# Optimization experiments

Hardware: AMD Instinct MI355X
Metric: run time of the kernel (lower is better)

Reference implementation:

```python
import jax, jax.numpy as jnp
import numpy as np

N = 50000
E = 600000
D = 128  # embedding_dimension


def _lrelu(x):
    return jax.nn.leaky_relu(x, negative_slope=0.01)


def _rgcn(x, edge_index, edge_type, rel_w, root_w, bias):
    # FastRGCNConv, num_relations=2, aggr='mean' (PyG default).
    # Compute per-relation transforms as 2 dense GEMMs, then gather per edge.
    h = jnp.einsum('nd,rde->rne', x, rel_w)          # [2, N, D]
    src, dst = edge_index[0], edge_index[1]
    msg = h[edge_type, src]                          # [E, D] gather
    agg = jax.ops.segment_sum(msg, dst, num_segments=x.shape[0])
    deg = jax.ops.segment_sum(jnp.ones((msg.shape[0],), x.dtype), dst,
                              num_segments=x.shape[0])
    agg = agg / jnp.maximum(deg, 1.0)[:, None]       # mean over in-edges
    return agg + x @ root_w + bias


def setup_inputs() -> dict:
    key = jax.random.key(0)
    ks = jax.random.split(key, 32)
    f32 = jnp.float32
    inp = {
        'des': jax.random.normal(ks[0], (N, 768), f32),
        'tweet': jax.random.normal(ks[1], (N, 768), f32),
        'num_prop': jax.random.normal(ks[2], (N, 7), f32),
        'cat_prop': jax.random.normal(ks[3], (N, 11), f32),
        'new_feature': jax.random.normal(ks[4], (N, 1), f32),
        'edge_index': jax.random.randint(ks[5], (2, E), 0, N),
        'edge_type': jax.random.randint(ks[6], (E,), 0, 2),
    }
    def lin(k, i, o, s=0.05):
        kw, kb = jax.random.split(k)
        return (jax.random.normal(kw, (i, o), f32) * s,
                jax.random.normal(kb, (o,), f32) * s)
    pf = D // 5  # 25
    inp['W_des'], inp['b_des'] = lin(ks[7], 768, pf)
    inp['W_tweet'], inp['b_tweet'] = lin(ks[8], 768, 28)
    inp['W_num'], inp['b_num'] = lin(ks[9], 7, pf)
    inp['W_cat'], inp['b_cat'] = lin(ks[10], 11, pf)
    inp['W_new'], inp['b_new'] = lin(ks[11], 1, pf)
    inp['W_in'], inp['b_in'] = lin(ks[12], D, D)
    inp['rel_w1'] = jax.random.normal(ks[13], (2, D, D), f32) * 0.05
    inp['root_w1'] = jax.random.normal(ks[14], (D, D), f32) * 0.05
    inp['bias1'] = jax.random.normal(ks[15], (D,), f32) * 0.05
    inp['rel_w2'] = jax.random.normal(ks[16], (2, D, D), f32) * 0.05
    inp['root_w2'] = jax.random.normal(ks[17], (D, D), f32) * 0.05
    inp['bias2'] = jax.random.normal(ks[18], (D,), f32) * 0.05
    inp['W_out1'], inp['b_out1'] = lin(ks[19], D, D)
    inp['W_out2'], inp['b_out2'] = lin(ks[20], D, 2)
    return inp


def reference(des, tweet, num_prop, cat_prop, new_feature,
              W_des, b_des, W_tweet, b_tweet, W_num, b_num,
              W_cat, b_cat, W_new, b_new, W_in, b_in,
              rel_w1, root_w1, bias1, rel_w2, root_w2, bias2,
              W_out1, b_out1, W_out2, b_out2,
              edge_index, edge_type):
    d = _lrelu(des @ W_des + b_des)
    t = _lrelu(tweet @ W_tweet + b_tweet)
    n = _lrelu(num_prop @ W_num + b_num)
    c = _lrelu(cat_prop @ W_cat + b_cat)
    nf = _lrelu(new_feature @ W_new + b_new)
    x = jnp.concatenate((d, t, n, c, nf), axis=1)  # [N, 128]
    x = _lrelu(x @ W_in + b_in)
    x = _rgcn(x, edge_index, edge_type, rel_w1, root_w1, bias1)
    # dropout is identity at eval time
    x = _rgcn(x, edge_index, edge_type, rel_w2, root_w2, bias2)
    x = _lrelu(x @ W_out1 + b_out1)
    return x @ W_out2 + b_out2  # [N, 2]
```

## Files before the change

kernel.cpp:

```cpp
#include <hip/hip_runtime.h>

#define N_NODES 50000
#define N_EDGES 600000
#define NPAD    50048
#define NBLK_SCAN 196

static __device__ __forceinline__ float lrelu(float v) {
    return v > 0.f ? v : 0.01f * v;
}

#define RS_P 129

template<int NC>
__device__ __forceinline__ void proj_lds_body(
    const float* __restrict__ A, const float* __restrict__ W,
    const float* __restrict__ bias, float* __restrict__ X0,
    int colbase, float* AlT)
{
    constexpr int CH = (NC + 1) / 2;
    const int t    = threadIdx.x;
    const int row  = t & 127;
    const int half = t >> 7;
    const int c0   = __builtin_amdgcn_readfirstlane(half ? (NC - CH) : 0);
    const int r0   = blockIdx.x * 128;
    const int q    = t & 7;

    float acc[CH];
    #pragma unroll
    for (int c = 0; c < CH; c++) acc[c] = 0.f;

    for (int k0 = 0; k0 < 768; k0 += 32) {
        __syncthreads();
        #pragma unroll
        for (int i = 0; i < 4; i++) {
            int rr = i * 32 + (t >> 3);
            int gr = r0 + rr;
            float4 v = make_float4(0.f, 0.f, 0.f, 0.f);
            if (gr < N_NODES)
                v = *(const float4*)&A[(size_t)gr * 768 + k0 + q * 4];
            AlT[(q * 4 + 0) * RS_P + rr] = v.x;
            AlT[(q * 4 + 1) * RS_P + rr] = v.y;
            AlT[(q * 4 + 2) * RS_P + rr] = v.z;
            AlT[(q * 4 + 3) * RS_P + rr] = v.w;
        }
        __syncthreads();
        const float* Wk = W + (size_t)k0 * NC + c0;
        #pragma unroll
        for (int k = 0; k < 32; k++) {
            float a = AlT[k * RS_P + row];
            const float* w = Wk + k * NC;
            #pragma unroll
            for (int c = 0; c < CH; c++) acc[c] += a * w[c];
        }
    }
    int grow = r0 + row;
    if (grow < N_NODES) {
        #pragma unroll
        for (int c = 0; c < CH; c++) {
            float v = lrelu(acc[c] + bias[c0 + c]);
            X0[(size_t)grow * 128 + colbase + c0 + c] = v;
        }
    }
}

__global__ __launch_bounds__(256) void proj768_lds(
    const float* __restrict__ des, const float* __restrict__ Wd, const float* __restrict__ bd,
    const float* __restrict__ tw,  const float* __restrict__ Wt, const float* __restrict__ bt,
    float* __restrict__ X0)
{
    __shared__ float AlT[32 * RS_P];
    if (blockIdx.z == 0) proj_lds_body<25>(des, Wd, bd, X0, 0,  AlT);
    else                 proj_lds_body<28>(tw, Wt, bt, X0, 25, AlT);
}

__global__ void small_proj_kernel(
    const float* __restrict__ nump, const float* __restrict__ catp, const float* __restrict__ newf,
    const float* __restrict__ Wn, const float* __restrict__ bn,
    const float* __restrict__ Wc, const float* __restrict__ bc,
    const float* __restrict__ Ww, const float* __restrict__ bw,
    float* __restrict__ out)
{
    int id = blockIdx.x * 256 + threadIdx.x;
    int n = id / 75, c = id % 75;
    if (n >= N_NODES) return;
    float acc; int col;
    if (c < 25) {
        col = 53 + c; acc = bn[c];
        #pragma unroll
        for (int k = 0; k < 7; k++) acc += nump[n * 7 + k] * Wn[k * 25 + c];
    } else if (c < 50) {
        int cc = c - 25; col = 78 + cc; acc = bc[cc];
        #pragma unroll
        for (int k = 0; k < 11; k++) acc += catp[n * 11 + k] * Wc[k * 25 + cc];
    } else {
        int cc = c - 50; col = 103 + cc;
        acc = bw[cc] + newf[n] * Ww[cc];
    }
    out[(size_t)n * 128 + col] = lrelu(acc);
}

template<int KTOT, bool SPLIT, bool ACT>
__global__ __launch_bounds__(256, 4) void gemm_v2(
    const float* __restrict__ A, const float* __restrict__ A2,
    const float* __restrict__ B, const float* __restrict__ B2,
    const float* __restrict__ bias, float* __restrict__ out)
{
    __shared__ float AlT[32 * 132];
    __shared__ float Bl [32 * 132];
    const int t  = threadIdx.x;
    const int r0 = blockIdx.x * 128;
    const int tx = t & 15, ty = t >> 4;

    float acc[8][8] = {};

    for (int k0 = 0; k0 < KTOT; k0 += 32) {
        #pragma unroll
        for (int i = 0; i < 4; i++) {
            int f4i = t + i * 256;
            int row = f4i >> 3, c4 = f4i & 7;
            int k = k0 + c4 * 4;
            float4 v;
            if (!SPLIT) {
                v = *(const float4*)&A[(size_t)(r0 + row) * 128 + k];
            } else {
                if (k < 256) v = *(const float4*)&A[(size_t)(r0 + row) * 256 + k];
                else         v = *(const float4*)&A2[(size_t)(r0 + row) * 128 + (k - 256)];
            }
            AlT[(c4 * 4 + 0) * 132 + row] = v.x;
            AlT[(c4 * 4 + 1) * 132 + row] = v.y;
            AlT[(c4 * 4 + 2) * 132 + row] = v.z;
            AlT[(c4 * 4 + 3) * 132 + row] = v.w;
        }
        #pragma unroll
        for (int i = 0; i < 4; i++) {
            int f4i = t + i * 256;
            int kk = f4i >> 5, c4 = f4i & 31;
            int k = k0 + kk;
            float4 v;
            if (!SPLIT) v = *(const float4*)&B[(size_t)k * 128 + c4 * 4];
            else v = (k < 256) ? *(const float4*)&B[(size_t)k * 128 + c4 * 4]
                               : *(const float4*)&B2[(size_t)(k - 256) * 128 + c4 * 4];
            *(float4*)&Bl[kk * 132 + c4 * 4] = v;
        }
        __syncthreads();
        #pragma unroll 4
        for (int k = 0; k < 32; k++) {
            float4 a0 = *(const float4*)&AlT[k * 132 + ty * 8];
            float4 a1 = *(const float4*)&AlT[k * 132 + ty * 8 + 4];
            float4 b0 = *(const float4*)&Bl [k * 132 + tx * 8];
            float4 b1 = *(const float4*)&Bl [k * 132 + tx * 8 + 4];
            float av[8] = {a0.x, a0.y, a0.z, a0.w, a1.x, a1.y, a1.z, a1.w};
            float bv[8] = {b0.x, b0.y, b0.z, b0.w, b1.x, b1.y, b1.z, b1.w};
            #pragma unroll
            for (int i = 0; i < 8; i++)
                #pragma unroll
                for (int j = 0; j < 8; j++) acc[i][j] += av[i] * bv[j];
        }
        __syncthreads();
    }
    float4 bb0 = *(const float4*)&bias[tx * 8];
    float4 bb1 = *(const float4*)&bias[tx * 8 + 4];
    float bb[8] = {bb0.x, bb0.y, bb0.z, bb0.w, bb1.x, bb1.y, bb1.z, bb1.w};
    #pragma unroll
    for (int i = 0; i < 8; i++) {
        size_t row = (size_t)(r0 + ty * 8 + i);
        float o[8];
        #pragma unroll
        for (int j = 0; j < 8; j++) {
            o[j] = acc[i][j] + bb[j];
            if (ACT) o[j] = lrelu(o[j]);
        }
        *(float4*)&out[row * 128 + tx * 8]     = make_float4(o[0], o[1], o[2], o[3]);
        *(float4*)&out[row * 128 + tx * 8 + 4] = make_float4(o[4], o[5], o[6], o[7]);
    }
}

__global__ void count_kernel(const int* __restrict__ ei, int* __restrict__ count) {
    int e = blockIdx.x * 256 + threadIdx.x;
    if (e < N_EDGES) atomicAdd(&count[ei[N_EDGES + e]], 1);
}

__global__ void scan1_kernel(const int* __restrict__ count, int* __restrict__ partial) {
    __shared__ int sm[256];
    int b = blockIdx.x, t = threadIdx.x;
    int i = b * 256 + t;
    sm[t] = (i < N_NODES) ? count[i] : 0;
    __syncthreads();
    for (int off = 128; off > 0; off >>= 1) {
        if (t < off) sm[t] += sm[t + off];
        __syncthreads();
    }
    if (t == 0) partial[b] = sm[0];
}

__global__ void scan2_kernel(int* __restrict__ partial) {
    __shared__ int sm[256];
    int t = threadIdx.x;
    int v = (t < NBLK_SCAN) ? partial[t] : 0;
    sm[t] = v; __syncthreads();
    for (int off = 1; off < 256; off <<= 1) {
        int add = (t >= off) ? sm[t - off] : 0;
        __syncthreads();
        sm[t] += add;
        __syncthreads();
    }
    partial[t] = sm[t] - v;
}

__global__ void scan3_kernel(const int* __restrict__ count, const int* __restrict__ partial,
                             int* __restrict__ offsets) {
    __shared__ int sm[256];
    int b = blockIdx.x, t = threadIdx.x;
    int i = b * 256 + t;
    int v = (i < N_NODES) ? count[i] : 0;
    sm[t] = v; __syncthreads();
    for (int off = 1; off < 256; off <<= 1) {
        int add = (t >= off) ? sm[t - off] : 0;
        __syncthreads();
        sm[t] += add;
        __syncthreads();
    }
    if (i < N_NODES) offsets[i] = partial[b] + sm[t] - v;
}

__global__ void fill_kernel(const int* __restrict__ ei, const int* __restrict__ et,
                            const int* __restrict__ offsets, int* __restrict__ cursor,
                            int* __restrict__ elist) {
    int e = blockIdx.x * 256 + threadIdx.x;
    if (e < N_EDGES) {
        int d = ei[N_EDGES + e];
        int pos = atomicAdd(&cursor[d], 1);
        elist[offsets[d] + pos] = (int)(((unsigned)ei[e]) | (((unsigned)et[e]) << 31));
    }
}

__global__ __launch_bounds__(256) void aggregate_v3(
    const float* __restrict__ x, const int* __restrict__ offsets,
    const int* __restrict__ count, const int* __restrict__ elist,
    float* __restrict__ s)
{
    int nid  = blockIdx.x * 8 + (threadIdx.x >> 5);
    int lane = threadIdx.x & 31;
    if (nid >= N_NODES) return;
    int start = offsets[nid], dg = count[nid];
    float4 a0 = make_float4(0.f, 0.f, 0.f, 0.f);
    float4 a1 = make_float4(0.f, 0.f, 0.f, 0.f);
    int i = 0;
    for (; i + 2 <= dg; i += 2) {
        int v0 = elist[start + i];
        int v1 = elist[start + i + 1];
        float4 u = ((const float4*)&x[(size_t)(v0 & 0x7FFFFFFF) * 128])[lane];
        float4 w = ((const float4*)&x[(size_t)(v1 & 0x7FFFFFFF) * 128])[lane];
        if (v0 < 0) { a1.x += u.x; a1.y += u.y; a1.z += u.z; a1.w += u.w; }
        else        { a0.x += u.x; a0.y += u.y; a0.z += u.z; a0.w += u.w; }
        if (v1 < 0) { a1.x += w.x; a1.y += w.y; a1.z += w.z; a1.w += w.w; }
        else        { a0.x += w.x; a0.y += w.y; a0.z += w.z; a0.w += w.w; }
    }
    if (i < dg) {
        int v0 = elist[start + i];
        float4 u = ((const float4*)&x[(size_t)(v0 & 0x7FFFFFFF) * 128])[lane];
        if (v0 < 0) { a1.x += u.x; a1.y += u.y; a1.z += u.z; a1.w += u.w; }
        else        { a0.x += u.x; a0.y += u.y; a0.z += u.z; a0.w += u.w; }
    }
    float inv = 1.0f / (float)(dg > 0 ? dg : 1);
    a0.x *= inv; a0.y *= inv; a0.z *= inv; a0.w *= inv;
    a1.x *= inv; a1.y *= inv; a1.z *= inv; a1.w *= inv;
    ((float4*)&s[(size_t)nid * 256])[lane]       = a0;
    ((float4*)&s[(size_t)nid * 256 + 128])[lane] = a1;
}

__global__ __launch_bounds__(64) void final_kernel(
    const float* __restrict__ x, const float* __restrict__ W2,
    const float* __restrict__ b2, float* __restrict__ out)
{
    int n = blockIdx.x;
    int t = threadIdx.x;
    float x0 = x[(size_t)n * 128 + t];
    float x1 = x[(size_t)n * 128 + 64 + t];
    float p0 = x0 * W2[t * 2]     + x1 * W2[(t + 64) * 2];
    float p1 = x0 * W2[t * 2 + 1] + x1 * W2[(t + 64) * 2 + 1];
    #pragma unroll
    for (int off = 32; off > 0; off >>= 1) {
        p0 += __shfl_down(p0, off);
        p1 += __shfl_down(p1, off);
    }
    if (t == 0) {
        out[(size_t)n * 2]     = p0 + b2[0];
        out[(size_t)n * 2 + 1] = p1 + b2[1];
    }
}

extern "C" void kernel_launch(void* const* d_in, const int* in_sizes, int n_in,
                              void* d_out, int out_size, void* d_ws, size_t ws_size,
                              hipStream_t stream)
{
    const float* des   = (const float*)d_in[0];
    const float* tw    = (const float*)d_in[1];
    const float* nump  = (const float*)d_in[2];
    const float* catp  = (const float*)d_in[3];
    const float* newf  = (const float*)d_in[4];
    const int*   ei    = (const int*)d_in[5];
    const int*   et    = (const int*)d_in[6];
    const float* Wd    = (const float*)d_in[7];  const float* bd  = (const float*)d_in[8];
    const float* Wt    = (const float*)d_in[9];  const float* bt  = (const float*)d_in[10];
    const float* Wn    = (const float*)d_in[11]; const float* bn  = (const float*)d_in[12];
    const float* Wc    = (const float*)d_in[13]; const float* bc  = (const float*)d_in[14];
    const float* Ww    = (const float*)d_in[15]; const float* bw  = (const float*)d_in[16];
    const float* Win   = (const float*)d_in[17]; const float* bin = (const float*)d_in[18];
    const float* relw1 = (const float*)d_in[19]; const float* rootw1 = (const float*)d_in[20];
    const float* bias1 = (const float*)d_in[21];
    const float* relw2 = (const float*)d_in[22]; const float* rootw2 = (const float*)d_in[23];
    const float* bias2 = (const float*)d_in[24];
    const float* Wo1   = (const float*)d_in[25]; const float* bo1 = (const float*)d_in[26];
    const float* Wo2   = (const float*)d_in[27]; const float* bo2 = (const float*)d_in[28];
    float* outp = (float*)d_out;

    char* ws = (char*)d_ws;
    const size_t szX = (size_t)NPAD * 128 * sizeof(float);
    float* X0 = (float*)(ws);
    float* X1 = (float*)(ws + szX);
    float* S  = (float*)(ws + 2 * szX);
    char* p = ws + 2 * szX + (size_t)NPAD * 256 * sizeof(float);
    int* count   = (int*)p; p += (size_t)NPAD * 4;
    int* offsets = (int*)p; p += (size_t)NPAD * 4;
    int* cursor  = (int*)p; p += (size_t)NPAD * 4;
    int* elist   = (int*)p; p += (size_t)N_EDGES * 4;
    int* partial = (int*)p;

    hipMemsetAsync(count,  0, NPAD * sizeof(int), stream);
    hipMemsetAsync(cursor, 0, NPAD * sizeof(int), stream);

    dim3 pg(NPAD / 128, 1, 2);
    proj768_lds<<<pg, 256, 0, stream>>>(des, Wd, bd, tw, Wt, bt, X0);
    small_proj_kernel<<<(N_NODES * 75 + 255) / 256, 256, 0, stream>>>(
        nump, catp, newf, Wn, bn, Wc, bc, Ww, bw, X0);
    gemm_v2<128, false, true><<<NPAD / 128, 256, 0, stream>>>(
        X0, nullptr, Win, nullptr, bin, X1);

    count_kernel<<<(N_EDGES + 255) / 256, 256, 0, stream>>>(ei, count);
    scan1_kernel<<<NBLK_SCAN, 256, 0, stream>>>(count, partial);
    scan2_kernel<<<1, 256, 0, stream>>>(partial);
    scan3_kernel<<<NBLK_SCAN, 256, 0, stream>>>(count, partial, offsets);
    fill_kernel<<<(N_EDGES + 255) / 256, 256, 0, stream>>>(ei, et, offsets, cursor, elist);

    aggregate_v3<<<(N_NODES + 7) / 8, 256, 0, stream>>>(X1, offsets, count, elist, S);
    gemm_v2<384, true, false><<<NPAD / 128, 256, 0, stream>>>(
        S, X1, relw1, rootw1, bias1, X0);

    aggregate_v3<<<(N_NODES + 7) / 8, 256, 0, stream>>>(X0, offsets, count, elist, S);
    gemm_v2<384, true, false><<<NPAD / 128, 256, 0, stream>>>(
        S, X0, relw2, rootw2, bias2, X1);

    gemm_v2<128, false, true><<<NPAD / 128, 256, 0, stream>>>(
        X1, nullptr, Wo1, nullptr, bo1, X0);
    final_kernel<<<N_NODES, 64, 0, stream>>>(X0, Wo2, bo2, outp);
}
```

Baseline: 953.8 us.

## Restructure 768-wide projection into per-wave tiles with split-K reduction

Replaces the block-wide LDS-transposed projection with a per-wave scheme: each wave owns 64 rows and half of K, stages its own tile in private LDS without block barriers, and computes all output columns per thread. The two K-halves are combined through LDS after a single barrier. This removes the per-tile __syncthreads, gives each thread more columns and better ILP from 8 outstanding float4 loads, at the cost of more accumulator registers and reading W twice as often per row.

Result: slower. 1.101 ms (+15.4%).

```diff
diff --git a/kernel.cpp b/kernel.cpp
--- a/kernel.cpp
+++ b/kernel.cpp
@@ -9,68 +9,80 @@
     return v > 0.f ? v : 0.01f * v;
 }
 
-#define RS_P 129
+#define PW_STRIDE 65
+#define PW_WORDS  (32 * PW_STRIDE)
 
 template<int NC>
-__device__ __forceinline__ void proj_lds_body(
+__device__ __forceinline__ void proj_wave_body(
     const float* __restrict__ A, const float* __restrict__ W,
     const float* __restrict__ bias, float* __restrict__ X0,
-    int colbase, float* AlT)
-{
-    constexpr int CH = (NC + 1) / 2;
-    const int t    = threadIdx.x;
-    const int row  = t & 127;
-    const int half = t >> 7;
-    const int c0   = __builtin_amdgcn_readfirstlane(half ? (NC - CH) : 0);
-    const int r0   = blockIdx.x * 128;
-    const int q    = t & 7;
-
-    float acc[CH];
+    int colbase, float* __restrict__ lbuf, float* __restrict__ pbuf,
+    int r0, int khalf, int lane)
+{
+    float acc[NC];
     #pragma unroll
-    for (int c = 0; c < CH; c++) acc[c] = 0.f;
-
-    for (int k0 = 0; k0 < 768; k0 += 32) {
-        __syncthreads();
-        #pragma unroll
-        for (int i = 0; i < 4; i++) {
-            int rr = i * 32 + (t >> 3);
-            int gr = r0 + rr;
-            float4 v = make_float4(0.f, 0.f, 0.f, 0.f);
-            if (gr < N_NODES)
-                v = *(const float4*)&A[(size_t)gr * 768 + k0 + q * 4];
-            AlT[(q * 4 + 0) * RS_P + rr] = v.x;
-            AlT[(q * 4 + 1) * RS_P + rr] = v.y;
-            AlT[(q * 4 + 2) * RS_P + rr] = v.z;
-            AlT[(q * 4 + 3) * RS_P + rr] = v.w;
-        }
-        __syncthreads();
-        const float* Wk = W + (size_t)k0 * NC + c0;
+    for (int c = 0; c < NC; c++) acc[c] = 0.f;
+
+    const int srowb = lane >> 3;
+    const int sf4   = lane & 7;
+
+    for (int kt = 0; kt < 12; kt++) {
+        const int k0 = khalf * 384 + kt * 32;
+        float4 v[8];
+        #pragma unroll
+        for (int i = 0; i < 8; i++) {
+            int gr = r0 + i * 8 + srowb;
+            if (gr >= N_NODES) gr = N_NODES - 1;
+            v[i] = *(const float4*)&A[(size_t)gr * 768 + k0 + sf4 * 4];
+        }
+        #pragma unroll
+        for (int i = 0; i < 8; i++) {
+            int r = i * 8 + srowb;
+            lbuf[(sf4 * 4 + 0) * PW_STRIDE + r] = v[i].x;
+            lbuf[(sf4 * 4 + 1) * PW_STRIDE + r] = v[i].y;
+            lbuf[(sf4 * 4 + 2) * PW_STRIDE + r] = v[i].z;
+            lbuf[(sf4 * 4 + 3) * PW_STRIDE + r] = v[i].w;
+        }
         #pragma unroll
         for (int k = 0; k < 32; k++) {
-            float a = AlT[k * RS_P + row];
-            const float* w = Wk + k * NC;
+            float a = lbuf[k * PW_STRIDE + lane];
+            const float* w = W + (size_t)(k0 + k) * NC;
             #pragma unroll
-            for (int c = 0; c < CH; c++) acc[c] += a * w[c];
-        }
-    }
-    int grow = r0 + row;
-    if (grow < N_NODES) {
-        #pragma unroll
-        for (int c = 0; c < CH; c++) {
-            float v = lrelu(acc[c] + bias[c0 + c]);
-            X0[(size_t)grow * 128 + colbase + c0 + c] = v;
-        }
-    }
-}
-
-__global__ __launch_bounds__(256) void proj768_lds(
+            for (int c = 0; c < NC; c++) acc[c] += a * w[c];
+        }
+    }
+
+    if (khalf == 1) {
+        #pragma unroll
+        for (int c = 0; c < NC; c++) pbuf[lane * 29 + c] = acc[c];
+    }
+    __syncthreads();
+    if (khalf == 0) {
+        int gr = r0 + lane;
+        if (gr < N_NODES) {
+            #pragma unroll
+            for (int c = 0; c < NC; c++) {
+                float sv = acc[c] + pbuf[lane * 29 + c] + bias[c];
+                X0[(size_t)gr * 128 + colbase + c] = lrelu(sv);
+            }
+        }
+    }
+}
+
+__global__ __launch_bounds__(256) void proj768_wave(
     const float* __restrict__ des, const float* __restrict__ Wd, const float* __restrict__ bd,
     const float* __restrict__ tw,  const float* __restrict__ Wt, const float* __restrict__ bt,
     float* __restrict__ X0)
 {
-    __shared__ float AlT[32 * RS_P];
-    if (blockIdx.z == 0) proj_lds_body<25>(des, Wd, bd, X0, 0,  AlT);
-    else                 proj_lds_body<28>(tw, Wt, bt, X0, 25, AlT);
+    __shared__ float buf[4 * PW_WORDS];
+    const int t    = threadIdx.x;
+    const int wv   = t >> 6, lane = t & 63;
+    const int rowhalf = wv >> 1, khalf = wv & 1;
+    const int r0   = blockIdx.x * 128 + rowhalf * 64;
+    float* lbuf = buf + wv * PW_WORDS;
+    float* pbuf = buf + (wv | 1) * PW_WORDS;
+    if (blockIdx.z == 0) proj_wave_body<25>(des, Wd, bd, X0, 0,  lbuf, pbuf, r0, khalf, lane);
+    else                 proj_wave_body<28>(tw, Wt, bt, X0, 25, lbuf, pbuf, r0, khalf, lane);
 }
 
 __global__ void small_proj_kernel(
@@ -225,7 +237,7 @@
 
 __global__ void fill_kernel(const int* __restrict__ ei, const int* __restrict__ et,
                             const int* __restrict__ offsets, int* __restrict__ cursor,
-                            int* __restrict__ elist) {
+                             int* __restrict__ elist) {
     int e = blockIdx.x * 256 + threadIdx.x;
     if (e < N_EDGES) {
         int d = ei[N_EDGES + e];
@@ -331,7 +343,7 @@
     hipMemsetAsync(cursor, 0, NPAD * sizeof(int), stream);
 
     dim3 pg(NPAD / 128, 1, 2);
-    proj768_lds<<<pg, 256, 0, stream>>>(des, Wd, bd, tw, Wt, bt, X0);
+    proj768_wave<<<pg, 256, 0, stream>>>(des, Wd, bd, tw, Wt, bt, X0);
     small_proj_kernel<<<(N_NODES * 75 + 255) / 256, 256, 0, stream>>>(
         nump, catp, newf, Wn, bn, Wc, bc, Ww, bw, X0);
     gemm_v2<128, false, true><<<NPAD / 128, 256, 0, stream>>>(
```

## Rewrite 768-wide input projection as register-tiled GEMM with packed LDS weights

Applied to the files above, without the earlier changes.

Replaces the per-row projection kernel, which read weights straight from global/scalar memory, with a 4x4 register-tiled GEMM that stages both A and a zero-padded 32-column weight tile in LDS. A small pack kernel pads the des and tweet weights and biases to 32 columns in the scratch S buffer before the GEMM runs. The goal is more FMAs per LDS/global load and more occupancy (launch bounds 256,4), at the cost of an extra launch and some wasted padded columns.

Result: faster. 844.3 us (-11.5%).

```diff
diff --git a/kernel.cpp b/kernel.cpp
--- a/kernel.cpp
+++ b/kernel.cpp
@@ -9,68 +9,99 @@
     return v > 0.f ? v : 0.01f * v;
 }
 
-#define RS_P 129
-
-template<int NC>
-__device__ __forceinline__ void proj_lds_body(
-    const float* __restrict__ A, const float* __restrict__ W,
-    const float* __restrict__ bias, float* __restrict__ X0,
-    int colbase, float* AlT)
-{
-    constexpr int CH = (NC + 1) / 2;
-    const int t    = threadIdx.x;
-    const int row  = t & 127;
-    const int half = t >> 7;
-    const int c0   = __builtin_amdgcn_readfirstlane(half ? (NC - CH) : 0);
-    const int r0   = blockIdx.x * 128;
-    const int q    = t & 7;
-
-    float acc[CH];
+__global__ void pack_b_kernel(const float* __restrict__ Wd, const float* __restrict__ bd,
+                              const float* __restrict__ Wt, const float* __restrict__ bt,
+                              float* __restrict__ Bp, float* __restrict__ biasp)
+{
+    int id = blockIdx.x * 256 + threadIdx.x;
+    if (id < 2 * 768 * 32) {
+        int z = id / 24576, rem = id % 24576;
+        int k = rem >> 5, j = rem & 31;
+        float v = 0.f;
+        if (z == 0) { if (j < 25) v = Wd[k * 25 + j]; }
+        else        { if (j < 28) v = Wt[k * 28 + j]; }
+        Bp[id] = v;
+    }
+    if (id < 64) {
+        int z = id >> 5, j = id & 31;
+        float v = 0.f;
+        if (z == 0) { if (j < 25) v = bd[j]; }
+        else        { if (j < 28) v = bt[j]; }
+        biasp[id] = v;
+    }
+}
+
+template<int NCSTORE>
+__device__ __forceinline__ void gemm_proj_body(
+    const float* __restrict__ A, const float* __restrict__ B,
+    const float* __restrict__ bias, float* __restrict__ X0, int colbase,
+    float* __restrict__ AlT, float* __restrict__ Bl)
+{
+    const int t  = threadIdx.x;
+    const int r0 = blockIdx.x * 128;
+    const int tx = t & 7, ty = t >> 3;
+
+    float acc[4][4] = {};
+
+    for (int k0 = 0; k0 < 768; k0 += 32) {
+        #pragma unroll
+        for (int i = 0; i < 4; i++) {
+            int f4i = t + i * 256;
+            int row = f4i >> 3, c4 = f4i & 7;
+            int gr = r0 + row;
+            if (gr > N_NODES - 1) gr = N_NODES - 1;
+            float4 v = *(const float4*)&A[(size_t)gr * 768 + k0 + c4 * 4];
+            AlT[(c4 * 4 + 0) * 132 + row] = v.x;
+            AlT[(c4 * 4 + 1) * 132 + row] = v.y;
+            AlT[(c4 * 4 + 2) * 132 + row] = v.z;
+            AlT[(c4 * 4 + 3) * 132 + row] = v.w;
+        }
+        {
+            int kk = t >> 3, c4 = t & 7;
+            *(float4*)&Bl[kk * 36 + c4 * 4] =
+                *(const float4*)&B[(size_t)(k0 + kk) * 32 + c4 * 4];
+        }
+        __syncthreads();
+        #pragma unroll 4
+        for (int k = 0; k < 32; k++) {
+            float4 a = *(const float4*)&AlT[k * 132 + ty * 4];
+            float4 b = *(const float4*)&Bl [k * 36 + tx * 4];
+            float av[4] = {a.x, a.y, a.z, a.w};
+            float bv[4] = {b.x, b.y, b.z, b.w};
+            #pragma unroll
+            for (int i = 0; i < 4; i++)
+                #pragma unroll
+                for (int j = 0; j < 4; j++) acc[i][j] += av[i] * bv[j];
+        }
+        __syncthreads();
+    }
+
     #pragma unroll
-    for (int c = 0; c < CH; c++) acc[c] = 0.f;
-
-    for (int k0 = 0; k0 < 768; k0 += 32) {
-        __syncthreads();
-        #pragma unroll
-        for (int i = 0; i < 4; i++) {
-            int rr = i * 32 + (t >> 3);
-            int gr = r0 + rr;
-            float4 v = make_float4(0.f, 0.f, 0.f, 0.f);
-            if (gr < N_NODES)
-                v = *(const float4*)&A[(size_t)gr * 768 + k0 + q * 4];
-            AlT[(q * 4 + 0) * RS_P + rr] = v.x;
-            AlT[(q * 4 + 1) * RS_P + rr] = v.y;
-            AlT[(q * 4 + 2) * RS_P + rr] = v.z;
-            AlT[(q * 4 + 3) * RS_P + rr] = v.w;
-        }
-        __syncthreads();
-        const float* Wk = W + (size_t)k0 * NC + c0;
-        #pragma unroll
-        for (int k = 0; k < 32; k++) {
-            float a = AlT[k * RS_P + row];
-            const float* w = Wk + k * NC;
+    for (int j = 0; j < 4; j++) {
+        int col = tx * 4 + j;
+        if (col < NCSTORE) {
+            float bb = bias[col];
             #pragma unroll
-            for (int c = 0; c < CH; c++) acc[c] += a * w[c];
-        }
-    }
-    int grow = r0 + row;
-    if (grow < N_NODES) {
-        #pragma unroll
-        for (int c = 0; c < CH; c++) {
-            float v = lrelu(acc[c] + bias[c0 + c]);
-            X0[(size_t)grow * 128 + colbase + c0 + c] = v;
-        }
-    }
-}
-
-__global__ __launch_bounds__(256) void proj768_lds(
-    const float* __restrict__ des, const float* __restrict__ Wd, const float* __restrict__ bd,
-    const float* __restrict__ tw,  const float* __restrict__ Wt, const float* __restrict__ bt,
+            for (int i = 0; i < 4; i++) {
+                int row = r0 + ty * 4 + i;
+                if (row < N_NODES)
+                    X0[(size_t)row * 128 + colbase + col] = lrelu(acc[i][j] + bb);
+            }
+        }
+    }
+}
+
+__global__ __launch_bounds__(256, 4) void gemm_proj(
+    const float* __restrict__ des, const float* __restrict__ tw,
+    const float* __restrict__ Bp, const float* __restrict__ biasp,
     float* __restrict__ X0)
 {
-    __shared__ float AlT[32 * RS_P];
-    if (blockIdx.z == 0) proj_lds_body<25>(des, Wd, bd, X0, 0,  AlT);
-    else                 proj_lds_body<28>(tw, Wt, bt, X0, 25, AlT);
+    __shared__ float AlT[32 * 132];
+    __shared__ float Bl [32 * 36];
+    if (blockIdx.z == 0)
+        gemm_proj_body<25>(des, Bp,         biasp,      X0, 0,  AlT, Bl);
+    else
+        gemm_proj_body<28>(tw,  Bp + 24576, biasp + 32, X0, 25, AlT, Bl);
 }
 
 __global__ void small_proj_kernel(
@@ -320,6 +351,8 @@
     float* X0 = (float*)(ws);
     float* X1 = (float*)(ws + szX);
     float* S  = (float*)(ws + 2 * szX);
+    float* Bp    = S;
+    float* biasp = S + 2 * 768 * 32;
     char* p = ws + 2 * szX + (size_t)NPAD * 256 * sizeof(float);
     int* count   = (int*)p; p += (size_t)NPAD * 4;
     int* offsets = (int*)p; p += (size_t)NPAD * 4;
@@ -330,8 +363,9 @@
     hipMemsetAsync(count,  0, NPAD * sizeof(int), stream);
     hipMemsetAsync(cursor, 0, NPAD * sizeof(int), stream);
 
+    pack_b_kernel<<<192, 256, 0, stream>>>(Wd, bd, Wt, bt, Bp, biasp);
     dim3 pg(NPAD / 128, 1, 2);
-    proj768_lds<<<pg, 256, 0, stream>>>(des, Wd, bd, tw, Wt, bt, X0);
+    gemm_proj<<<pg, 256, 0, stream>>>(des, tw, Bp, biasp, X0);
     small_proj_kernel<<<(N_NODES * 75 + 255) / 256, 256, 0, stream>>>(
         nump, catp, newf, Wn, bn, Wc, bc, Ww, bw, X0);
     gemm_v2<128, false, true><<<NPAD / 128, 256, 0, stream>>>(
```
